# Kernel tuning notes

Measured on AMD Instinct MI355X. Metric: run time of the kernel, lower is better.

## Reference

```python
import jax, jax.numpy as jnp
import numpy as np

B, N, H, T = 128, 512, 128, 32


def setup_inputs() -> dict:
    key = jax.random.key(0)
    ks = jax.random.split(key, 6)
    s = 0.05  # small init scale keeps softmax logits sane
    return {
        "encoder_outputs": jax.random.normal(ks[0], (B, N, H), jnp.float32),
        "W_ih": jax.random.normal(ks[1], (4 * H, H), jnp.float32) * s,
        "W_hh": jax.random.normal(ks[2], (4 * H, H), jnp.float32) * s,
        "b_ih": jnp.zeros((4 * H,), jnp.float32),
        "b_hh": jnp.zeros((4 * H,), jnp.float32),
        "W1": jax.random.normal(ks[3], (H, H), jnp.float32) * s,
        "W2": jax.random.normal(ks[4], (H, H), jnp.float32) * s,
        "v": jax.random.normal(ks[5], (H,), jnp.float32) * s,
        "decode_steps": T,
    }


def reference(encoder_outputs, W_ih, W_hh, b_ih, b_hh, W1, W2, v, decode_steps):
    b, n, h = encoder_outputs.shape
    dtype = encoder_outputs.dtype
    # W1(encoder_outputs) is loop-invariant: hoist it (same math as the torch loop)
    enc_trans = jnp.einsum("bnh,kh->bnk", encoder_outputs, W1)  # [B,n,H]

    dec0 = encoder_outputs.mean(axis=1)  # [B,H]
    hx0 = jnp.zeros((b, h), dtype)
    cx0 = jnp.zeros((b, h), dtype)
    mask0 = jnp.zeros((b, n), bool)
    key0 = jax.random.key(42)
    rows = jnp.arange(b)

    def step(carry, _):
        dec_input, hx, cx, mask, key = carry
        # torch.nn.LSTMCell: gates ordered i, f, g, o
        gates = dec_input @ W_ih.T + b_ih + hx @ W_hh.T + b_hh  # [B,4H]
        i, f, g, o = jnp.split(gates, 4, axis=-1)
        i = jax.nn.sigmoid(i)
        f = jax.nn.sigmoid(f)
        g = jnp.tanh(g)
        o = jax.nn.sigmoid(o)
        cx_new = f * cx + i * g
        hx_new = o * jnp.tanh(cx_new)
        # additive attention scores
        dec_trans = hx_new @ W2.T  # [B,H]
        scores = jnp.einsum("bnh,h->bn", jnp.tanh(enc_trans + dec_trans[:, None, :]), v)
        scores = jnp.where(mask, -jnp.inf, scores)  # masked_fill(-inf)
        # sample next node (torch.multinomial on softmax == categorical on logits)
        key, sub = jax.random.split(key)
        idx = jax.random.categorical(sub, scores, axis=-1)  # [B]
        probs = jax.nn.softmax(scores, axis=-1)
        sel_log_prob = jnp.log(jnp.take_along_axis(probs, idx[:, None], axis=1)[:, 0] + 1e-9)
        mask_new = mask.at[rows, idx].set(True)
        dec_next = jnp.take_along_axis(encoder_outputs, idx[:, None, None], axis=1)[:, 0]  # [B,H]
        return (dec_next, hx_new, cx_new, mask_new, key), (idx, sel_log_prob)

    _, (tours, log_probs) = jax.lax.scan(
        step, (dec0, hx0, cx0, mask0, key0), xs=None, length=decode_steps
    )
    return tours.T, log_probs.T  # [B,T], [B,T]
```

## Files before the change

### kernel.cpp

```cpp
#include <hip/hip_runtime.h>
#include <cstdint>
#include <cstddef>


constexpr int B = 128, N = 512, H = 128, T = 32;
constexpr int G4 = 4 * H;
constexpr float TINYF = 1.17549435e-38f;

__host__ __device__ inline uint32_t rotl32(uint32_t v, int d) {
  return (v << d) | (v >> (32 - d));
}

__host__ __device__ inline void tf2x32(uint32_t k0, uint32_t k1,
                                       uint32_t x0, uint32_t x1,
                                       uint32_t& o0, uint32_t& o1) {
  uint32_t ks2 = k0 ^ k1 ^ 0x1BD11BDAu;
  x0 += k0; x1 += k1;
#define TF_R(r) x0 += x1; x1 = rotl32(x1, (r)); x1 ^= x0;
  TF_R(13) TF_R(15) TF_R(26) TF_R(6)
  x0 += k1; x1 += ks2 + 1u;
  TF_R(17) TF_R(29) TF_R(16) TF_R(24)
  x0 += ks2; x1 += k0 + 2u;
  TF_R(13) TF_R(15) TF_R(26) TF_R(6)
  x0 += k0; x1 += k1 + 3u;
  TF_R(17) TF_R(29) TF_R(16) TF_R(24)
  x0 += k1; x1 += ks2 + 4u;
  TF_R(13) TF_R(15) TF_R(26) TF_R(6)
  x0 += ks2; x1 += k0 + 5u;
#undef TF_R
  o0 = x0; o1 = x1;
}

struct KeyArgs { uint32_t k[2 * T]; };

static KeyArgs make_subkeys() {
  KeyArgs ka;
  uint32_t k0 = 0u, k1 = 42u;
  for (int t = 0; t < T; ++t) {
    uint32_t n0, n1, s0, s1;
    tf2x32(k0, k1, 0u, 0u, n0, n1);
    tf2x32(k0, k1, 0u, 1u, s0, s1);
    ka.k[2 * t] = s0; ka.k[2 * t + 1] = s1;
    k0 = n0; k1 = n1;
  }
  return ka;
}

__device__ inline uint32_t gumbel_bits(uint32_t sk0, uint32_t sk1, int i) {
  uint32_t o0, o1;
  tf2x32(sk0, sk1, 0u, (uint32_t)i, o0, o1);
  return o0 ^ o1;
}

__device__ inline float fast_tanh(float x) {
  float cx = fminf(9.0f, fmaxf(-9.0f, x));
  float t = __expf(2.0f * cx);
  return (t - 1.0f) * __builtin_amdgcn_rcpf(t + 1.0f);
}

__global__ __launch_bounds__(256) void k_setup(
    const float* __restrict__ enc, const float* __restrict__ W1,
    const float* __restrict__ Wih, const float* __restrict__ Whh,
    const float* __restrict__ W2,
    float* __restrict__ encT2, float* __restrict__ WihT,
    float* __restrict__ WhhT, float* __restrict__ W2T) {
  __shared__ float w1t[128 * 129];
  __shared__ __align__(16) float es[16 * 128];

  if (blockIdx.x >= 4096) {
    int base = (blockIdx.x - 4096) * 256 + threadIdx.x;
    const int stride = 64 * 256;
    for (int i = base; i < H * G4; i += stride) {
      int h = i >> 9, j = i & (G4 - 1);
      WihT[i] = Wih[j * H + h];
      WhhT[i] = Whh[j * H + h];
    }
    for (int i = base; i < H * H; i += stride) {
      int h = i >> 7, k = i & (H - 1);
      W2T[i] = W2[k * H + h];
    }
    return;
  }
  for (int i = threadIdx.x; i < H * H; i += 256) {
    int k = i >> 7, h = i & 127;
    w1t[h * 129 + k] = W1[i];
  }
  int blk = blockIdx.x;
  int b = blk >> 5;
  int n0 = (blk & 31) << 4;
  const float* src = enc + ((size_t)b * N + n0) * H;
  for (int i = threadIdx.x; i < 16 * 128; i += 256) es[i] = src[i];
  __syncthreads();
  int k = threadIdx.x & 127, ng = threadIdx.x >> 7;
  float acc[8] = {0.f, 0.f, 0.f, 0.f, 0.f, 0.f, 0.f, 0.f};
  for (int h = 0; h < H; h += 4) {
    float w0 = w1t[(h + 0) * 129 + k];
    float w1 = w1t[(h + 1) * 129 + k];
    float w2 = w1t[(h + 2) * 129 + k];
    float w3 = w1t[(h + 3) * 129 + k];
#pragma unroll
    for (int j = 0; j < 8; ++j) {
      const float4 e = *(const float4*)&es[(ng * 8 + j) * 128 + h];
      acc[j] += w0 * e.x + w1 * e.y + w2 * e.z + w3 * e.w;
    }
  }
  float* dst = encT2 + (size_t)b * H * N + (size_t)k * N + n0 + ng * 8;
  ((float4*)dst)[0] = make_float4(acc[0], acc[1], acc[2], acc[3]);
  ((float4*)dst)[1] = make_float4(acc[4], acc[5], acc[6], acc[7]);
}

__global__ __launch_bounds__(1024, 4) void k_decode(
    const float* __restrict__ enc, const float* __restrict__ encT2,
    const float* __restrict__ WihT, const float* __restrict__ WhhT,
    const float* __restrict__ W2T,
    const float* __restrict__ bih, const float* __restrict__ bhh,
    const float* __restrict__ v,
    KeyArgs keys, float* __restrict__ out) {
  __shared__ float2 xh[H];
  __shared__ float cs[H];
  __shared__ float2 dv[H];
  __shared__ __align__(16) float bsum[G4];
  __shared__ float pg[2][G4];
  __shared__ float pdt[4][H];
  __shared__ float ps[2][N];
  __shared__ float sc[N];
  __shared__ float gb[T * N];
  __shared__ float wr_z[8], wr_s[8];
  __shared__ int wr_i[8];
  __shared__ float outb[2][T];

  const int tid = threadIdx.x;
  const int b = blockIdx.x;
  const int lane = tid & 63;
  const int wave = tid >> 6;
  const int kh = tid >> 9;
  const int nn = tid & 511;

  if (tid < 512) {
    int h = tid & 127, part = tid >> 7;
    float s = 0.f;
    const float* p = enc + ((size_t)b * N + part * 128) * H + h;
#pragma unroll 8
    for (int n = 0; n < 128; ++n) s += p[(size_t)n * H];
    pdt[part][h] = s;
    bsum[tid] = bih[tid] + bhh[tid];
  }
#pragma unroll
  for (int q = 0; q < 16; ++q) {
    int idx = q * 1024 + tid;
    int tt = idx >> 9, n = idx & 511;
    uint32_t bits = gumbel_bits(keys.k[2 * tt], keys.k[2 * tt + 1], b * N + n);
    float f = __uint_as_float((bits >> 9) | 0x3f800000u) - 1.0f;
    float u = fmaxf(TINYF, f + TINYF);
    gb[tt * N + n] = -logf(-logf(u));
  }
  if (tid < 128) { cs[tid] = 0.f; dv[tid] = make_float2(0.f, v[tid]); }
  float er[64];
  {
    const float* ep = encT2 + (size_t)b * (H * N) + (size_t)(kh * 64) * N + nn;
#pragma unroll
    for (int kk = 0; kk < 64; ++kk) er[kk] = ep[(size_t)kk * N];
  }
  __syncthreads();
  if (tid < 128)
    xh[tid] = make_float2(
        (pdt[0][tid] + pdt[1][tid] + pdt[2][tid] + pdt[3][tid]) * (1.0f / N), 0.f);
  bool masked = false;
  __syncthreads();

  for (int t = 0; t < T; ++t) {
    {
      const int hb = kh * 64;
      const float* wi = WihT + (size_t)hb * G4 + nn;
      const float* wh = WhhT + (size_t)hb * G4 + nn;
      float a0 = 0.f, a1 = 0.f;
#pragma unroll 8
      for (int h = 0; h < 64; ++h) {
        float2 xhv = xh[hb + h];
        a0 += wi[h * G4] * xhv.x;
        a1 += wh[h * G4] * xhv.y;
      }
      pg[kh][nn] = a0 + a1;
    }
    __syncthreads();
    if (tid < 128) {
      float gi = pg[0][tid] + pg[1][tid] + bsum[tid];
      float gf = pg[0][H + tid] + pg[1][H + tid] + bsum[H + tid];
      float gg = pg[0][2 * H + tid] + pg[1][2 * H + tid] + bsum[2 * H + tid];
      float go = pg[0][3 * H + tid] + pg[1][3 * H + tid] + bsum[3 * H + tid];
      gi = 1.0f / (1.0f + expf(-gi));
      gf = 1.0f / (1.0f + expf(-gf));
      gg = tanhf(gg);
      go = 1.0f / (1.0f + expf(-go));
      float c = gf * cs[tid] + gi * gg;
      cs[tid] = c;
      xh[tid].y = go * tanhf(c);
    }
    __syncthreads();
    if (tid < 512) {
      int k = tid & 127, part = tid >> 7;
      const float* w2 = W2T + (size_t)(part * 32) * H + k;
      const int hb = part * 32;
      float a = 0.f;
#pragma unroll 8
      for (int h = 0; h < 32; ++h) a += w2[h * H] * xh[hb + h].y;
      pdt[part][k] = a;
    }
    __syncthreads();
    if (tid < 128)
      dv[tid].x = pdt[0][tid] + pdt[1][tid] + pdt[2][tid] + pdt[3][tid];
    __syncthreads();
    {
      const int kb = kh * 64;
      float a0 = 0.f, a1 = 0.f;
#pragma unroll
      for (int kk = 0; kk < 64; kk += 2) {
        float2 d0 = dv[kb + kk];
        float2 d1 = dv[kb + kk + 1];
        a0 += d0.y * fast_tanh(er[kk] + d0.x);
        a1 += d1.y * fast_tanh(er[kk + 1] + d1.x);
      }
      ps[kh][nn] = a0 + a1;
    }
    __syncthreads();
    if (tid < 512) {
      float s = masked ? -INFINITY : (ps[0][tid] + ps[1][tid]);
      sc[tid] = s;
      float z = s + gb[t * N + tid];
      int zi = tid;
#pragma unroll
      for (int d = 32; d >= 1; d >>= 1) {
        float oz = __shfl_xor(z, d);
        int oi = __shfl_xor(zi, d);
        if (oz > z || (oz == z && oi < zi)) { z = oz; zi = oi; }
      }
      float e = expf(s);
#pragma unroll
      for (int d = 32; d >= 1; d >>= 1) e += __shfl_xor(e, d);
      if (lane == 0) { wr_z[wave] = z; wr_i[wave] = zi; wr_s[wave] = e; }
    }
    __syncthreads();
    {
      float bz = wr_z[0]; int bi = wr_i[0];
#pragma unroll
      for (int w = 1; w < 8; ++w) {
        float wz = wr_z[w]; int wj = wr_i[w];
        if (wz > bz || (wz == bz && wj < bi)) { bz = wz; bi = wj; }
      }
      if (tid == bi) masked = true;
      if (tid >= 512 && tid < 640)
        xh[tid - 512].x = enc[((size_t)b * N + bi) * H + (tid - 512)];
      if (tid == 0) {
        float S = ((((((wr_s[0] + wr_s[1]) + wr_s[2]) + wr_s[3]) + wr_s[4])
                    + wr_s[5]) + wr_s[6]) + wr_s[7];
        float p = expf(sc[bi]) / S;
        outb[0][t] = (float)bi;
        outb[1][t] = logf(p + 1e-9f);
      }
    }
    __syncthreads();
  }
  if (tid < T) {
    out[(size_t)b * T + tid] = outb[0][tid];
    out[(size_t)B * T + (size_t)b * T + tid] = outb[1][tid];
  }
}

extern "C" void kernel_launch(void* const* d_in, const int* in_sizes, int n_in,
                              void* d_out, int out_size, void* d_ws, size_t ws_size,
                              hipStream_t stream) {
  (void)in_sizes; (void)n_in; (void)out_size; (void)ws_size;
  const float* enc = (const float*)d_in[0];
  const float* Wih = (const float*)d_in[1];
  const float* Whh = (const float*)d_in[2];
  const float* bih = (const float*)d_in[3];
  const float* bhh = (const float*)d_in[4];
  const float* W1  = (const float*)d_in[5];
  const float* W2  = (const float*)d_in[6];
  const float* v   = (const float*)d_in[7];
  float* out = (float*)d_out;
  float* ws = (float*)d_ws;

  float* WihT  = ws;
  float* WhhT  = ws + 65536;
  float* W2T   = ws + 131072;
  float* encT2 = ws + 147456;

  KeyArgs keys = make_subkeys();

  k_setup<<<4160, 256, 0, stream>>>(enc, W1, Wih, Whh, W2, encT2, WihT, WhhT, W2T);
  k_decode<<<B, 1024, 0, stream>>>(enc, encT2, WihT, WhhT, W2T, bih, bhh, v,
                                   keys, out);
}
```

Measured before the change: 628.7 us.

## Split each batch row across two blocks with inter-block flag handshake

The decode kernel now runs two 512-thread blocks per batch row, each covering half of the 512 nodes. The halves exchange their argmax candidate and partial softmax sum through global memory slots guarded by release/acquire flags and a spin-wait. The aim is to use more CUs and shrink each block's per-step latency. Alongside this, the Gumbel noise is computed inline each step instead of being precomputed into shared memory, the LSTM gate GEMV uses float4 weight loads, and the W2 projection is fused into a single wave. The spin handshake relies on both blocks of a pair being resident at the same time and adds a cross-CU round trip every step. The setup kernel also changes, reading the encoder directly from global memory with larger tiles instead of staging it in shared memory.

```diff
diff --git a/kernel.cpp b/kernel.cpp
--- a/kernel.cpp
+++ b/kernel.cpp
@@ -6,6 +6,7 @@
 constexpr int B = 128, N = 512, H = 128, T = 32;
 constexpr int G4 = 4 * H;
 constexpr float TINYF = 1.17549435e-38f;
+constexpr uint32_t FLAG_BASE = 0x5AFE0000u;
 
 __host__ __device__ inline uint32_t rotl32(uint32_t v, int d) {
   return (v << d) | (v >> (32 - d));
@@ -58,18 +59,26 @@
   return (t - 1.0f) * __builtin_amdgcn_rcpf(t + 1.0f);
 }
 
-__global__ __launch_bounds__(256) void k_setup(
+__device__ inline void ag_store(uint32_t* p, uint32_t v) {
+  __hip_atomic_store(p, v, __ATOMIC_RELAXED, __HIP_MEMORY_SCOPE_AGENT);
+}
+__device__ inline uint32_t ag_load(const uint32_t* p) {
+  return __hip_atomic_load(p, __ATOMIC_RELAXED, __HIP_MEMORY_SCOPE_AGENT);
+}
+
+__global__ __launch_bounds__(512) void k_setup(
     const float* __restrict__ enc, const float* __restrict__ W1,
     const float* __restrict__ Wih, const float* __restrict__ Whh,
     const float* __restrict__ W2,
     float* __restrict__ encT2, float* __restrict__ WihT,
-    float* __restrict__ WhhT, float* __restrict__ W2T) {
+    float* __restrict__ WhhT, float* __restrict__ W2T,
+    uint32_t* __restrict__ slots) {
   __shared__ float w1t[128 * 129];
-  __shared__ __align__(16) float es[16 * 128];
-
-  if (blockIdx.x >= 4096) {
-    int base = (blockIdx.x - 4096) * 256 + threadIdx.x;
-    const int stride = 64 * 256;
+
+  const int tid = threadIdx.x;
+  if (blockIdx.x >= 1024) {
+    int base = (blockIdx.x - 1024) * 512 + tid;
+    const int stride = 64 * 512;
     for (int i = base; i < H * G4; i += stride) {
       int h = i >> 9, j = i & (G4 - 1);
       WihT[i] = Wih[j * H + h];
@@ -79,85 +88,80 @@
       int h = i >> 7, k = i & (H - 1);
       W2T[i] = W2[k * H + h];
     }
+    for (int i = base; i < 2048; i += stride) slots[i] = 0u;
     return;
   }
-  for (int i = threadIdx.x; i < H * H; i += 256) {
+  for (int i = tid; i < H * H; i += 512) {
     int k = i >> 7, h = i & 127;
     w1t[h * 129 + k] = W1[i];
   }
-  int blk = blockIdx.x;
-  int b = blk >> 5;
-  int n0 = (blk & 31) << 4;
-  const float* src = enc + ((size_t)b * N + n0) * H;
-  for (int i = threadIdx.x; i < 16 * 128; i += 256) es[i] = src[i];
   __syncthreads();
-  int k = threadIdx.x & 127, ng = threadIdx.x >> 7;
-  float acc[8] = {0.f, 0.f, 0.f, 0.f, 0.f, 0.f, 0.f, 0.f};
+  const int b = blockIdx.x >> 3;
+  const int n0 = (blockIdx.x & 7) << 6;
+  const int k = tid & 127, ng = tid >> 7;
+  const float* encb = enc + ((size_t)b * N + n0 + ng * 16) * H;
+  float acc[16];
+#pragma unroll
+  for (int j = 0; j < 16; ++j) acc[j] = 0.f;
   for (int h = 0; h < H; h += 4) {
     float w0 = w1t[(h + 0) * 129 + k];
     float w1 = w1t[(h + 1) * 129 + k];
     float w2 = w1t[(h + 2) * 129 + k];
     float w3 = w1t[(h + 3) * 129 + k];
 #pragma unroll
-    for (int j = 0; j < 8; ++j) {
-      const float4 e = *(const float4*)&es[(ng * 8 + j) * 128 + h];
+    for (int j = 0; j < 16; ++j) {
+      const float4 e = *(const float4*)(encb + (size_t)j * H + h);
       acc[j] += w0 * e.x + w1 * e.y + w2 * e.z + w3 * e.w;
     }
   }
-  float* dst = encT2 + (size_t)b * H * N + (size_t)k * N + n0 + ng * 8;
-  ((float4*)dst)[0] = make_float4(acc[0], acc[1], acc[2], acc[3]);
-  ((float4*)dst)[1] = make_float4(acc[4], acc[5], acc[6], acc[7]);
-}
-
-__global__ __launch_bounds__(1024, 4) void k_decode(
+  float* dst = encT2 + (size_t)b * H * N + (size_t)k * N + n0 + ng * 16;
+#pragma unroll
+  for (int q = 0; q < 4; ++q)
+    ((float4*)dst)[q] = make_float4(acc[4 * q], acc[4 * q + 1],
+                                    acc[4 * q + 2], acc[4 * q + 3]);
+}
+
+__global__ __launch_bounds__(512) void k_decode(
     const float* __restrict__ enc, const float* __restrict__ encT2,
     const float* __restrict__ WihT, const float* __restrict__ WhhT,
     const float* __restrict__ W2T,
     const float* __restrict__ bih, const float* __restrict__ bhh,
     const float* __restrict__ v,
-    KeyArgs keys, float* __restrict__ out) {
+    KeyArgs keys, uint32_t* __restrict__ slots, float* __restrict__ out) {
   __shared__ float2 xh[H];
   __shared__ float cs[H];
   __shared__ float2 dv[H];
   __shared__ __align__(16) float bsum[G4];
-  __shared__ float pg[2][G4];
+  __shared__ __align__(16) float p1arr[2][2][G4];
   __shared__ float pdt[4][H];
-  __shared__ float ps[2][N];
-  __shared__ float sc[N];
-  __shared__ float gb[T * N];
-  __shared__ float wr_z[8], wr_s[8];
-  __shared__ int wr_i[8];
+  __shared__ float ps[2][256];
+  __shared__ float sc[256];
+  __shared__ float wr_z[4], wr_s[4];
+  __shared__ int wr_i[4];
+  __shared__ int s_idx;
   __shared__ float outb[2][T];
 
   const int tid = threadIdx.x;
-  const int b = blockIdx.x;
+  const int bq = blockIdx.x & 127;
+  const int nh = blockIdx.x >> 7;
   const int lane = tid & 63;
   const int wave = tid >> 6;
-  const int kh = tid >> 9;
-  const int nn = tid & 511;
-
-  if (tid < 512) {
+
+  {
     int h = tid & 127, part = tid >> 7;
     float s = 0.f;
-    const float* p = enc + ((size_t)b * N + part * 128) * H + h;
+    const float* p = enc + ((size_t)bq * N + part * 128) * H + h;
 #pragma unroll 8
     for (int n = 0; n < 128; ++n) s += p[(size_t)n * H];
     pdt[part][h] = s;
     bsum[tid] = bih[tid] + bhh[tid];
   }
-#pragma unroll
-  for (int q = 0; q < 16; ++q) {
-    int idx = q * 1024 + tid;
-    int tt = idx >> 9, n = idx & 511;
-    uint32_t bits = gumbel_bits(keys.k[2 * tt], keys.k[2 * tt + 1], b * N + n);
-    float f = __uint_as_float((bits >> 9) | 0x3f800000u) - 1.0f;
-    float u = fmaxf(TINYF, f + TINYF);
-    gb[tt * N + n] = -logf(-logf(u));
-  }
   if (tid < 128) { cs[tid] = 0.f; dv[tid] = make_float2(0.f, v[tid]); }
   float er[64];
   {
-    const float* ep = encT2 + (size_t)b * (H * N) + (size_t)(kh * 64) * N + nn;
+    const int kh = tid >> 8, nn = tid & 255;
+    const float* ep = encT2 + (size_t)bq * (H * N) + (size_t)(kh * 64) * N
+                      + nh * 256 + nn;
 #pragma unroll
     for (int kk = 0; kk < 64; ++kk) er[kk] = ep[(size_t)kk * N];
   }
@@ -168,49 +172,67 @@
   bool masked = false;
   __syncthreads();
 
+  uint32_t* my = slots + (((size_t)nh * 128 + bq) << 3);
+  uint32_t* th = slots + (((size_t)(nh ^ 1) * 128 + bq) << 3);
+
   for (int t = 0; t < T; ++t) {
     {
-      const int hb = kh * 64;
-      const float* wi = WihT + (size_t)hb * G4 + nn;
-      const float* wh = WhhT + (size_t)hb * G4 + nn;
-      float a0 = 0.f, a1 = 0.f;
+      const int j4 = tid & 127, hh = (tid >> 7) & 1, m = tid >> 8;
+      const float* WT = m ? WhhT : WihT;
+      const float4* w4 = (const float4*)(WT + (size_t)(hh * 64) * G4) + j4;
+      float a0 = 0.f, a1 = 0.f, a2 = 0.f, a3 = 0.f;
 #pragma unroll 8
       for (int h = 0; h < 64; ++h) {
-        float2 xhv = xh[hb + h];
-        a0 += wi[h * G4] * xhv.x;
-        a1 += wh[h * G4] * xhv.y;
-      }
-      pg[kh][nn] = a0 + a1;
-    }
-    __syncthreads();
-    if (tid < 128) {
-      float gi = pg[0][tid] + pg[1][tid] + bsum[tid];
-      float gf = pg[0][H + tid] + pg[1][H + tid] + bsum[H + tid];
-      float gg = pg[0][2 * H + tid] + pg[1][2 * H + tid] + bsum[2 * H + tid];
-      float go = pg[0][3 * H + tid] + pg[1][3 * H + tid] + bsum[3 * H + tid];
-      gi = 1.0f / (1.0f + expf(-gi));
-      gf = 1.0f / (1.0f + expf(-gf));
-      gg = tanhf(gg);
-      go = 1.0f / (1.0f + expf(-go));
-      float c = gf * cs[tid] + gi * gg;
-      cs[tid] = c;
-      xh[tid].y = go * tanhf(c);
-    }
-    __syncthreads();
-    if (tid < 512) {
-      int k = tid & 127, part = tid >> 7;
-      const float* w2 = W2T + (size_t)(part * 32) * H + k;
-      const int hb = part * 32;
-      float a = 0.f;
+        float4 w = w4[h * 128];
+        float2 xv = xh[hh * 64 + h];
+        float x = m ? xv.y : xv.x;
+        a0 += w.x * x; a1 += w.y * x; a2 += w.z * x; a3 += w.w * x;
+      }
+      ((float4*)&p1arr[m][hh][0])[j4] = make_float4(a0, a1, a2, a3);
+    }
+    __syncthreads();
+    if (wave == 0) {
+#pragma unroll
+      for (int hh2 = 0; hh2 < 2; ++hh2) {
+        const int h = hh2 * 64 + lane;
+        float gi = (p1arr[0][0][h] + p1arr[1][0][h])
+                 + (p1arr[0][1][h] + p1arr[1][1][h]) + bsum[h];
+        float gf = (p1arr[0][0][H + h] + p1arr[1][0][H + h])
+                 + (p1arr[0][1][H + h] + p1arr[1][1][H + h]) + bsum[H + h];
+        float gg = (p1arr[0][0][2 * H + h] + p1arr[1][0][2 * H + h])
+                 + (p1arr[0][1][2 * H + h] + p1arr[1][1][2 * H + h]) + bsum[2 * H + h];
+        float go = (p1arr[0][0][3 * H + h] + p1arr[1][0][3 * H + h])
+                 + (p1arr[0][1][3 * H + h] + p1arr[1][1][3 * H + h]) + bsum[3 * H + h];
+        gi = 1.0f / (1.0f + expf(-gi));
+        gf = 1.0f / (1.0f + expf(-gf));
+        gg = tanhf(gg);
+        go = 1.0f / (1.0f + expf(-go));
+        float c = gf * cs[h] + gi * gg;
+        cs[h] = c;
+        xh[h].y = go * tanhf(c);
+      }
+      __asm__ __volatile__("s_waitcnt lgkmcnt(0)" ::: "memory");
+      const int k2 = lane;
+      float q0[4], q1[4];
+#pragma unroll
+      for (int part = 0; part < 4; ++part) {
+        float u0 = 0.f, u1 = 0.f;
 #pragma unroll 8
-      for (int h = 0; h < 32; ++h) a += w2[h * H] * xh[hb + h].y;
-      pdt[part][k] = a;
-    }
-    __syncthreads();
-    if (tid < 128)
-      dv[tid].x = pdt[0][tid] + pdt[1][tid] + pdt[2][tid] + pdt[3][tid];
+        for (int h = 0; h < 32; ++h) {
+          const int hg = part * 32 + h;
+          float2 w2v = *(const float2*)&W2T[(size_t)hg * H + 2 * k2];
+          float hv = xh[hg].y;
+          u0 += w2v.x * hv;
+          u1 += w2v.y * hv;
+        }
+        q0[part] = u0; q1[part] = u1;
+      }
+      dv[2 * k2].x     = ((q0[0] + q0[1]) + q0[2]) + q0[3];
+      dv[2 * k2 + 1].x = ((q1[0] + q1[1]) + q1[2]) + q1[3];
+    }
     __syncthreads();
     {
+      const int kh = tid >> 8, nn = tid & 255;
       const int kb = kh * 64;
       float a0 = 0.f, a1 = 0.f;
 #pragma unroll
@@ -223,11 +245,16 @@
       ps[kh][nn] = a0 + a1;
     }
     __syncthreads();
-    if (tid < 512) {
+    if (tid < 256) {
+      const int ng = nh * 256 + tid;
       float s = masked ? -INFINITY : (ps[0][tid] + ps[1][tid]);
       sc[tid] = s;
-      float z = s + gb[t * N + tid];
-      int zi = tid;
+      uint32_t bits = gumbel_bits(keys.k[2 * t], keys.k[2 * t + 1], bq * N + ng);
+      float f = __uint_as_float((bits >> 9) | 0x3f800000u) - 1.0f;
+      float u = fmaxf(TINYF, f + TINYF);
+      float g = -logf(-logf(u));
+      float z = s + g;
+      int zi = ng;
 #pragma unroll
       for (int d = 32; d >= 1; d >>= 1) {
         float oz = __shfl_xor(z, d);
@@ -240,29 +267,48 @@
       if (lane == 0) { wr_z[wave] = z; wr_i[wave] = zi; wr_s[wave] = e; }
     }
     __syncthreads();
-    {
+    if (tid == 0) {
       float bz = wr_z[0]; int bi = wr_i[0];
 #pragma unroll
-      for (int w = 1; w < 8; ++w) {
-        float wz = wr_z[w]; int wj = wr_i[w];
-        if (wz > bz || (wz == bz && wj < bi)) { bz = wz; bi = wj; }
-      }
-      if (tid == bi) masked = true;
-      if (tid >= 512 && tid < 640)
-        xh[tid - 512].x = enc[((size_t)b * N + bi) * H + (tid - 512)];
-      if (tid == 0) {
-        float S = ((((((wr_s[0] + wr_s[1]) + wr_s[2]) + wr_s[3]) + wr_s[4])
-                    + wr_s[5]) + wr_s[6]) + wr_s[7];
-        float p = expf(sc[bi]) / S;
-        outb[0][t] = (float)bi;
+      for (int w = 1; w < 4; ++w) {
+        if (wr_z[w] > bz || (wr_z[w] == bz && wr_i[w] < bi)) { bz = wr_z[w]; bi = wr_i[w]; }
+      }
+      float es = ((wr_s[0] + wr_s[1]) + wr_s[2]) + wr_s[3];
+      float scat = sc[bi - nh * 256];
+      ag_store(my + 0, __float_as_uint(bz));
+      ag_store(my + 1, (uint32_t)bi);
+      ag_store(my + 2, __float_as_uint(es));
+      ag_store(my + 3, __float_as_uint(scat));
+      __hip_atomic_store(my + 7, FLAG_BASE + (uint32_t)t,
+                         __ATOMIC_RELEASE, __HIP_MEMORY_SCOPE_AGENT);
+      while (__hip_atomic_load(th + 7, __ATOMIC_ACQUIRE, __HIP_MEMORY_SCOPE_AGENT)
+             != FLAG_BASE + (uint32_t)t)
+        __builtin_amdgcn_s_sleep(1);
+      float oz = __uint_as_float(ag_load(th + 0));
+      int oi = (int)ag_load(th + 1);
+      float oes = __uint_as_float(ag_load(th + 2));
+      float oscat = __uint_as_float(ag_load(th + 3));
+      bool iwin = (bz > oz) || (bz == oz && bi < oi);
+      int idx = iwin ? bi : oi;
+      s_idx = idx;
+      if (nh == 0) {
+        float S = es + oes;
+        float p = expf(iwin ? scat : oscat) / S;
+        outb[0][t] = (float)idx;
         outb[1][t] = logf(p + 1e-9f);
       }
     }
     __syncthreads();
-  }
-  if (tid < T) {
-    out[(size_t)b * T + tid] = outb[0][tid];
-    out[(size_t)B * T + (size_t)b * T + tid] = outb[1][tid];
+    if (tid < 256) {
+      if (nh * 256 + tid == s_idx) masked = true;
+    } else if (tid < 384) {
+      xh[tid - 256].x = enc[((size_t)bq * N + s_idx) * H + (tid - 256)];
+    }
+    __syncthreads();
+  }
+  if (nh == 0 && tid < T) {
+    out[(size_t)bq * T + tid] = outb[0][tid];
+    out[(size_t)B * T + (size_t)bq * T + tid] = outb[1][tid];
   }
 }
 
@@ -284,11 +330,13 @@
   float* WihT  = ws;
   float* WhhT  = ws + 65536;
   float* W2T   = ws + 131072;
-  float* encT2 = ws + 147456;
+  uint32_t* slots = (uint32_t*)(ws + 147456);
+  float* encT2 = ws + 149504;
 
   KeyArgs keys = make_subkeys();
 
-  k_setup<<<4160, 256, 0, stream>>>(enc, W1, Wih, Whh, W2, encT2, WihT, WhhT, W2T);
-  k_decode<<<B, 1024, 0, stream>>>(enc, encT2, WihT, WhhT, W2T, bih, bhh, v,
-                                   keys, out);
-}
+  k_setup<<<1088, 512, 0, stream>>>(enc, W1, Wih, Whh, W2, encT2,
+                                    WihT, WhhT, W2T, slots);
+  k_decode<<<2 * B, 512, 0, stream>>>(enc, encT2, WihT, WhhT, W2T, bih, bhh, v,
+                                      keys, slots, out);
+}
```

New measurement: 1.000 ms. +59.1%, slower.

## Overlap recurrent W_hh gate matvec with sampling and split setup kernels

Applied to the files above, without the earlier changes.

The LSTM gate matvec is split in two. The W_ih part runs at step start on 512 threads using float2 loads. The W_hh part runs on the otherwise idle upper 512 threads during the argmax/softmax reduction phase, which takes it off the serial critical path. __syncthreads is replaced by a raw lgkmcnt-wait plus s_barrier, and the setup kernel is split into a transpose kernel and an encoder-projection kernel that reads W1T from global memory instead of staging W1 in LDS. The split setup adds a launch, and the raw barrier skips waiting on global memory ops (vmcnt), which could be fragile.

```diff
diff --git a/kernel.cpp b/kernel.cpp
--- a/kernel.cpp
+++ b/kernel.cpp
@@ -6,6 +6,8 @@
 constexpr int B = 128, N = 512, H = 128, T = 32;
 constexpr int G4 = 4 * H;
 constexpr float TINYF = 1.17549435e-38f;
+
+#define LBAR() __asm__ __volatile__("s_waitcnt lgkmcnt(0)\n\ts_barrier" ::: "memory")
 
 __host__ __device__ inline uint32_t rotl32(uint32_t v, int d) {
   return (v << d) | (v >> (32 - d));
@@ -58,33 +60,30 @@
   return (t - 1.0f) * __builtin_amdgcn_rcpf(t + 1.0f);
 }
 
-__global__ __launch_bounds__(256) void k_setup(
-    const float* __restrict__ enc, const float* __restrict__ W1,
-    const float* __restrict__ Wih, const float* __restrict__ Whh,
-    const float* __restrict__ W2,
-    float* __restrict__ encT2, float* __restrict__ WihT,
-    float* __restrict__ WhhT, float* __restrict__ W2T) {
-  __shared__ float w1t[128 * 129];
+__global__ void k_transpose(const float* __restrict__ Wih, const float* __restrict__ Whh,
+                            const float* __restrict__ W2, const float* __restrict__ W1,
+                            float* __restrict__ WihT, float* __restrict__ WhhT,
+                            float* __restrict__ W2T, float* __restrict__ W1T) {
+  int i = blockIdx.x * blockDim.x + threadIdx.x;
+  if (i < H * G4) {
+    int h = i >> 9, j = i & (G4 - 1);
+    WihT[i] = Wih[j * H + h];
+  } else if (i < 2 * H * G4) {
+    int q = i - H * G4; int h = q >> 9, j = q & (G4 - 1);
+    WhhT[q] = Whh[j * H + h];
+  } else if (i < 2 * H * G4 + H * H) {
+    int q = i - 2 * H * G4; int h = q >> 7, k = q & (H - 1);
+    W2T[q] = W2[k * H + h];
+  } else if (i < 2 * H * G4 + 2 * H * H) {
+    int q = i - 2 * H * G4 - H * H; int h = q >> 7, k = q & (H - 1);
+    W1T[q] = W1[k * H + h];
+  }
+}
+
+__global__ __launch_bounds__(256) void k_enc_trans(const float* __restrict__ enc,
+                                                   const float* __restrict__ W1T,
+                                                   float* __restrict__ encT2) {
   __shared__ __align__(16) float es[16 * 128];
-
-  if (blockIdx.x >= 4096) {
-    int base = (blockIdx.x - 4096) * 256 + threadIdx.x;
-    const int stride = 64 * 256;
-    for (int i = base; i < H * G4; i += stride) {
-      int h = i >> 9, j = i & (G4 - 1);
-      WihT[i] = Wih[j * H + h];
-      WhhT[i] = Whh[j * H + h];
-    }
-    for (int i = base; i < H * H; i += stride) {
-      int h = i >> 7, k = i & (H - 1);
-      W2T[i] = W2[k * H + h];
-    }
-    return;
-  }
-  for (int i = threadIdx.x; i < H * H; i += 256) {
-    int k = i >> 7, h = i & 127;
-    w1t[h * 129 + k] = W1[i];
-  }
   int blk = blockIdx.x;
   int b = blk >> 5;
   int n0 = (blk & 31) << 4;
@@ -94,10 +93,10 @@
   int k = threadIdx.x & 127, ng = threadIdx.x >> 7;
   float acc[8] = {0.f, 0.f, 0.f, 0.f, 0.f, 0.f, 0.f, 0.f};
   for (int h = 0; h < H; h += 4) {
-    float w0 = w1t[(h + 0) * 129 + k];
-    float w1 = w1t[(h + 1) * 129 + k];
-    float w2 = w1t[(h + 2) * 129 + k];
-    float w3 = w1t[(h + 3) * 129 + k];
+    float w0 = W1T[(h + 0) * H + k];
+    float w1 = W1T[(h + 1) * H + k];
+    float w2 = W1T[(h + 2) * H + k];
+    float w3 = W1T[(h + 3) * H + k];
 #pragma unroll
     for (int j = 0; j < 8; ++j) {
       const float4 e = *(const float4*)&es[(ng * 8 + j) * 128 + h];
@@ -120,7 +119,8 @@
   __shared__ float cs[H];
   __shared__ float2 dv[H];
   __shared__ __align__(16) float bsum[G4];
-  __shared__ float pg[2][G4];
+  __shared__ float pgx[2][G4];
+  __shared__ float pgh[2][G4];
   __shared__ float pdt[4][H];
   __shared__ float ps[2][N];
   __shared__ float sc[N];
@@ -145,6 +145,7 @@
     pdt[part][h] = s;
     bsum[tid] = bih[tid] + bhh[tid];
   }
+  ((float*)pgh)[tid] = 0.f;
 #pragma unroll
   for (int q = 0; q < 16; ++q) {
     int idx = q * 1024 + tid;
@@ -169,25 +170,28 @@
   __syncthreads();
 
   for (int t = 0; t < T; ++t) {
-    {
-      const int hb = kh * 64;
-      const float* wi = WihT + (size_t)hb * G4 + nn;
-      const float* wh = WhhT + (size_t)hb * G4 + nn;
+    if (tid < 512) {
+      const int j2 = tid & 255, hhf = tid >> 8;
+      const float2* w2p = (const float2*)(WihT + (size_t)(hhf * 64) * G4) + j2;
       float a0 = 0.f, a1 = 0.f;
 #pragma unroll 8
       for (int h = 0; h < 64; ++h) {
-        float2 xhv = xh[hb + h];
-        a0 += wi[h * G4] * xhv.x;
-        a1 += wh[h * G4] * xhv.y;
-      }
-      pg[kh][nn] = a0 + a1;
-    }
-    __syncthreads();
+        float2 w = w2p[h * 256];
+        float x = xh[hhf * 64 + h].x;
+        a0 += w.x * x; a1 += w.y * x;
+      }
+      ((float2*)&pgx[hhf][0])[j2] = make_float2(a0, a1);
+    }
+    LBAR();
     if (tid < 128) {
-      float gi = pg[0][tid] + pg[1][tid] + bsum[tid];
-      float gf = pg[0][H + tid] + pg[1][H + tid] + bsum[H + tid];
-      float gg = pg[0][2 * H + tid] + pg[1][2 * H + tid] + bsum[2 * H + tid];
-      float go = pg[0][3 * H + tid] + pg[1][3 * H + tid] + bsum[3 * H + tid];
+      float gi = (pgx[0][tid] + pgh[0][tid])
+               + (pgx[1][tid] + pgh[1][tid]) + bsum[tid];
+      float gf = (pgx[0][H + tid] + pgh[0][H + tid])
+               + (pgx[1][H + tid] + pgh[1][H + tid]) + bsum[H + tid];
+      float gg = (pgx[0][2 * H + tid] + pgh[0][2 * H + tid])
+               + (pgx[1][2 * H + tid] + pgh[1][2 * H + tid]) + bsum[2 * H + tid];
+      float go = (pgx[0][3 * H + tid] + pgh[0][3 * H + tid])
+               + (pgx[1][3 * H + tid] + pgh[1][3 * H + tid]) + bsum[3 * H + tid];
       gi = 1.0f / (1.0f + expf(-gi));
       gf = 1.0f / (1.0f + expf(-gf));
       gg = tanhf(gg);
@@ -196,7 +200,7 @@
       cs[tid] = c;
       xh[tid].y = go * tanhf(c);
     }
-    __syncthreads();
+    LBAR();
     if (tid < 512) {
       int k = tid & 127, part = tid >> 7;
       const float* w2 = W2T + (size_t)(part * 32) * H + k;
@@ -206,10 +210,10 @@
       for (int h = 0; h < 32; ++h) a += w2[h * H] * xh[hb + h].y;
       pdt[part][k] = a;
     }
-    __syncthreads();
+    LBAR();
     if (tid < 128)
       dv[tid].x = pdt[0][tid] + pdt[1][tid] + pdt[2][tid] + pdt[3][tid];
-    __syncthreads();
+    LBAR();
     {
       const int kb = kh * 64;
       float a0 = 0.f, a1 = 0.f;
@@ -222,7 +226,7 @@
       }
       ps[kh][nn] = a0 + a1;
     }
-    __syncthreads();
+    LBAR();
     if (tid < 512) {
       float s = masked ? -INFINITY : (ps[0][tid] + ps[1][tid]);
       sc[tid] = s;
@@ -238,8 +242,20 @@
 #pragma unroll
       for (int d = 32; d >= 1; d >>= 1) e += __shfl_xor(e, d);
       if (lane == 0) { wr_z[wave] = z; wr_i[wave] = zi; wr_s[wave] = e; }
-    }
-    __syncthreads();
+    } else {
+      const int u = tid - 512;
+      const int j2 = u & 255, hhf = u >> 8;
+      const float2* w2p = (const float2*)(WhhT + (size_t)(hhf * 64) * G4) + j2;
+      float a0 = 0.f, a1 = 0.f;
+#pragma unroll 8
+      for (int h = 0; h < 64; ++h) {
+        float2 w = w2p[h * 256];
+        float hv = xh[hhf * 64 + h].y;
+        a0 += w.x * hv; a1 += w.y * hv;
+      }
+      ((float2*)&pgh[hhf][0])[j2] = make_float2(a0, a1);
+    }
+    LBAR();
     {
       float bz = wr_z[0]; int bi = wr_i[0];
 #pragma unroll
@@ -258,7 +274,7 @@
         outb[1][t] = logf(p + 1e-9f);
       }
     }
-    __syncthreads();
+    LBAR();
   }
   if (tid < T) {
     out[(size_t)b * T + tid] = outb[0][tid];
@@ -284,11 +300,13 @@
   float* WihT  = ws;
   float* WhhT  = ws + 65536;
   float* W2T   = ws + 131072;
-  float* encT2 = ws + 147456;
+  float* W1T   = ws + 147456;
+  float* encT2 = ws + 163840;
 
   KeyArgs keys = make_subkeys();
 
-  k_setup<<<4160, 256, 0, stream>>>(enc, W1, Wih, Whh, W2, encT2, WihT, WhhT, W2T);
+  k_transpose<<<640, 256, 0, stream>>>(Wih, Whh, W2, W1, WihT, WhhT, W2T, W1T);
+  k_enc_trans<<<B * N / 16, 256, 0, stream>>>(enc, W1T, encT2);
   k_decode<<<B, 1024, 0, stream>>>(enc, encT2, WihT, WhhT, W2T, bih, bhh, v,
                                    keys, out);
 }
```

After: 772.6 us. +22.9%, slower.
